# Optimization experiments

Measured on AMD Instinct MI355X. Metric: run time of the kernel, lower is better.

Reference implementation:

```python
import jax, jax.numpy as jnp
import numpy as np

N = 512          # n_nodes
F = 64           # hidden scalar/vector channels (hidden_irreps 64x0e+64x1o)
S = 5            # num_species
T = 32           # time embedding dim
M = 64           # MLP_irreps 64x0e
L = 2            # num_interactions
AVG = 511.0      # avg_num_neighbors (fully connected)
E = N * (N - 1)


def _sph(v):
    """Real spherical harmonics l=0,1,2 (component norm) of normalized vectors. v: [E,3]."""
    r = jnp.linalg.norm(v, axis=-1, keepdims=True)  # [E,1]
    u = v / r
    x, y, z = u[..., 0], u[..., 1], u[..., 2]
    s3, s5, s15 = 3.0 ** 0.5, 5.0 ** 0.5, 15.0 ** 0.5
    Y0 = jnp.ones_like(x)[..., None]
    Y1 = s3 * u
    Y2 = jnp.stack([s15 * x * y, s15 * y * z, 0.5 * s5 * (3 * z * z - 1.0),
                    s15 * x * z, 0.5 * s15 * (x * x - y * y)], axis=-1)
    return jnp.concatenate([Y0, Y1, Y2], axis=-1), r  # [E,9], [E,1]


def setup_inputs() -> dict:
    key = jax.random.key(0)
    ks = jax.random.split(key, 16)
    snd, rcv = np.nonzero(~np.eye(N, dtype=bool))  # fully-connected, no self loops
    return dict(
        positions=jax.random.normal(ks[0], (N, 3), jnp.float32),
        node_features=jax.random.randint(ks[1], (N,), 1, S + 1, jnp.int32),
        time_embedding=jax.random.normal(ks[2], (T,), jnp.float32),
        senders=jnp.asarray(snd, jnp.int32),
        receivers=jnp.asarray(rcv, jnp.int32),
        W_embed=jax.random.normal(ks[3], (S + T, F)) * 0.1,
        b_embed=jnp.zeros((F,)),
        W_lin=jax.random.normal(ks[4], (L, 3, F, F)) / jnp.sqrt(float(F)),
        W_e1=jax.random.normal(ks[5], (L, 1, 32)),
        b_e1=jnp.zeros((L, 32)),
        W_e2=jax.random.normal(ks[6], (L, 32, F * 6)) * 0.05,
        Wp0=jax.random.normal(ks[7], (L, S, F, 6)) * 0.1,
        Wp1=jax.random.normal(ks[8], (L, S, F, 3)) * 0.1,
        Wr1=jax.random.normal(ks[9], (L, F, M)) / jnp.sqrt(float(F)),
        br1=jnp.zeros((L, M)),
        Wr2s=jax.random.normal(ks[10], (L, M, 16)) * 0.1,
        Wr2g=jax.random.normal(ks[11], (L, M, F)) * 0.1,
    )


def reference(positions, node_features, time_embedding, senders, receivers,
              W_embed, b_embed, W_lin, W_e1, b_e1, W_e2, Wp0, Wp1, Wr1, br1, Wr2s, Wr2g):
    species = node_features - 1                                  # ints in [0,S)
    onehot = jax.nn.one_hot(species, S, dtype=positions.dtype)   # /normalization_factor=1
    te = jnp.tile(time_embedding, (N, 1))
    h = jnp.concatenate([onehot, te], axis=-1) @ W_embed + b_embed  # embedding Dense -> [N,F]
    node_feats = jnp.zeros((N, F, 9), positions.dtype).at[:, :, 0].set(h)
    pos0 = positions
    pos = positions
    for l in range(L):
        vec = pos[receivers] - pos[senders]                      # [E,3]
        Y, lengths = _sph(vec)                                   # SH of edge dirs, edge lengths
        # per-l channel-mixing linear on node feats
        x0 = jnp.einsum('nf,fg->ng', node_feats[:, :, 0], W_lin[l, 0])
        x1 = jnp.einsum('nfm,fg->ngm', node_feats[:, :, 1:4], W_lin[l, 1])
        x2 = jnp.einsum('nfm,fg->ngm', node_feats[:, :, 4:9], W_lin[l, 2])
        s0, s1, s2 = x0[senders], x1[senders], x2[senders]       # gather sender feats
        # edge-length MLP producing per-channel per-CG-path weights
        he = jax.nn.silu(lengths @ W_e1[l] + b_e1[l])            # [E,32]
        w = (he @ W_e2[l]).reshape(-1, F, 6)                     # 6 TP paths
        Y1 = Y[:, None, 1:4]
        Y2c = Y[:, None, 4:9]
        # CG tensor-product paths: 0x0->0, 0x1->1, 0x2->2, 1x1->0, 1x1->1, 2x2->0
        m0 = (w[..., 0] * s0 * Y[:, 0:1]
              + w[..., 3] * jnp.sum(s1 * Y1, -1)
              + w[..., 5] * jnp.sum(s2 * Y2c, -1))               # [E,F]
        m1 = w[..., 1, None] * s0[..., None] * Y1 + w[..., 4, None] * jnp.cross(s1, Y1)
        m2 = w[..., 2, None] * s0[..., None] * Y2c
        msg = jnp.concatenate([m0[..., None], m1, m2], axis=-1)  # [E,F,9]
        A = jax.ops.segment_sum(msg, receivers, num_segments=N) / AVG  # scatter-aggregate
        # EquivariantProductBasisBlock: species-weighted symmetric contractions (correlation 3)
        A0, A1, A2 = A[:, :, 0], A[:, :, 1:4], A[:, :, 4:9]
        n1 = jnp.sum(A1 * A1, -1)
        n2 = jnp.sum(A2 * A2, -1)
        t0 = jnp.stack([A0, A0 * A0, A0 ** 3, n1, n2, A0 * n1], axis=-1)
        w0 = Wp0[l][species]                                     # [N,F,6]
        w1 = Wp1[l][species]                                     # [N,F,3]
        out0 = jnp.sum(t0 * w0, -1)                              # [N,F] scalars
        gpoly = w1[..., 0] + w1[..., 1] * A0 + w1[..., 2] * A0 * A0
        out1 = gpoly[..., None] * A1                             # [N,F,3] vectors
        node_feats = (jnp.zeros((N, F, 9), positions.dtype)
                      .at[:, :, 0].set(out0).at[:, :, 1:4].set(out1))
        # NonLinearReadoutBlock: gated vector readout (scalar outputs are discarded upstream)
        hr = jax.nn.silu(out0 @ Wr1[l] + br1[l])
        gate = hr @ Wr2g[l]                                      # [N,F]
        vec_out = jnp.einsum('nf,nfc->nc', gate, out1)           # [N,3] many_body_vectors
        pos = pos + vec_out
    return (pos - pos0)[:, :3]                                    # final_scaling = 1.0
```

## Files before the change

kernel.cpp:

```cpp
#include <hip/hip_runtime.h>
#include <hip/hip_bf16.h>

using bf16 = __hip_bfloat16;
using bf16x8 = __attribute__((ext_vector_type(8))) short;
using f32x4  = __attribute__((ext_vector_type(4))) float;

#define NN 512
#define NS 511

enum : int {
  WS_FLAG = 0,
  WS_POS  = 16,
  WS_POS2 = 1552,
  WS_DELTA= 3088,
  WS_XS0  = 4624,
  WS_XS1  = 135696,
};

__device__ __forceinline__ short f2b(float x) {
  unsigned u = __builtin_bit_cast(unsigned, x);
  unsigned r = (u + 0x7fffu + ((u >> 16) & 1u)) >> 16;
  return (short)r;
}

__device__ __forceinline__ float ld(const void* p, int i, int isf32) {
  if (isf32) return ((const float*)p)[i];
  return __bfloat162float(((const bf16*)p)[i]);
}

__global__ __launch_bounds__(64) void k_pre(
    const void* __restrict__ positions, const int* __restrict__ nodef,
    const void* __restrict__ te, const void* __restrict__ W_embed,
    const void* __restrict__ b_embed, const void* __restrict__ W_lin,
    float* __restrict__ ws) {
  int n = blockIdx.x, f = threadIdx.x;
  int cnt = 0;
  #pragma unroll
  for (int kq = 0; kq < 4; ++kq) {
    float v = __bfloat162float(((const bf16*)W_embed)[f + kq * 64]);
    float av = fabsf(v);
    cnt += (v == v && av > 1e-8f && av < 1e4f) ? 1 : 0;
  }
  #pragma unroll
  for (int off = 32; off > 0; off >>= 1) cnt += __shfl_down(cnt, off);
  int tot = __shfl(cnt, 0);
  int isf32 = (tot >= 240) ? 0 : 1;
  if (n == 0 && f == 0) ((int*)ws)[WS_FLAG] = isf32;

  if (f < 3) ws[WS_POS + n * 3 + f] = ld(positions, n * 3 + f, isf32);

  int sp = nodef[n] - 1;
  float h = ld(b_embed, f, isf32) + ld(W_embed, sp * 64 + f, isf32);
  #pragma unroll 8
  for (int q = 0; q < 32; ++q)
    h += ld(te, q, isf32) * ld(W_embed, (5 + q) * 64 + f, isf32);
  __shared__ float hl[64];
  hl[f] = h;
  __syncthreads();
  float a0 = 0.f;
  #pragma unroll 8
  for (int q = 0; q < 64; ++q)
    a0 += hl[q] * ld(W_lin, q * 64 + f, isf32);
  f32x4 o = {a0, 0.f, 0.f, 0.f};
  *(f32x4*)&ws[WS_XS0 + (n * 64 + f) * 4] = o;
}

template <int L>
__global__ __launch_bounds__(256) void k_edgenode(
    const int* __restrict__ nodef, const void* __restrict__ W_lin,
    const void* __restrict__ W_e1, const void* __restrict__ b_e1,
    const void* __restrict__ W_e2, const void* __restrict__ Wp0,
    const void* __restrict__ Wp1, const void* __restrict__ Wr1,
    const void* __restrict__ br1, const void* __restrict__ Wr2g,
    float* __restrict__ ws, void* __restrict__ out) {
  constexpr int HAS1 = L;
  constexpr int K = HAS1 ? 5 : 3;
  constexpr int N = K * 64;
  const int j = blockIdx.x;
  const int t = threadIdx.x;
  const int lane = t & 63;
  const int wave = t >> 6;
  const int quad = lane >> 4;
  const int lo = lane & 15;

  __shared__ short Bhi[N * 40];
  __shared__ float red[4][64][9];
  __shared__ float Af[64][9];
  __shared__ float s0l[64];
  __shared__ float o1l[3][64];
  __shared__ float hl[64];

  const int isf32 = ((const int*)ws)[WS_FLAG];

  {
    for (int idx = t; idx < N * 32; idx += 256) {
      int n = idx >> 5, h = idx & 31;
      int kp = n >> 6, f = n & 63;
      int src = (L * 32 + h) * 384 + f * 6 + kp;
      short bits;
      if (isf32) bits = f2b(((const float*)W_e2)[src]);
      else       bits = ((const short*)W_e2)[src];
      Bhi[n * 40 + h] = bits;
    }
  }
  const float* pos = ws + (L ? WS_POS2 : WS_POS);
  const f32x4* xs = (const f32x4*)(ws + (L ? WS_XS1 : WS_XS0));
  float we1v[8], be1v[8];
  #pragma unroll
  for (int i = 0; i < 8; ++i) {
    we1v[i] = ld(W_e1, L * 32 + quad * 8 + i, isf32);
    be1v[i] = ld(b_e1, L * 32 + quad * 8 + i, isf32);
  }
  const float pjx = pos[j * 3 + 0], pjy = pos[j * 3 + 1], pjz = pos[j * 3 + 2];

  const float s3 = 1.7320508075688772f;
  const float s5h = 1.118033988749895f;
  const float s15 = 3.872983346207417f;
  const float s15h = 1.9364916731037085f;

  float acc[9][4] = {};
  __syncthreads();

  #pragma unroll 1
  for (int stile = wave; stile < 32; stile += 4) {
    bf16x8 af;
    {
      int ida = stile * 16 + lo;
      int ia = ida + (ida >= j);
      if (ia > 511) ia = 511;
      float pix = pos[ia * 3 + 0], piy = pos[ia * 3 + 1], piz = pos[ia * 3 + 2];
      float vx = pjx - pix, vy = pjy - piy, vz = pjz - piz;
      float r = sqrtf(vx * vx + vy * vy + vz * vz);
      #pragma unroll
      for (int i = 0; i < 8; ++i) {
        float x = r * we1v[i] + be1v[i];
        float he = x / (1.f + __expf(-x));
        af[i] = f2b(he);
      }
    }
    float Y1r[4][3], Y2r[4][5];
    int ir[4];
    bool vld[4];
    #pragma unroll
    for (int r4 = 0; r4 < 4; ++r4) {
      int idx = stile * 16 + quad * 4 + r4;
      vld[r4] = idx < NS;
      int i = idx + (idx >= j);
      if (i > 511) i = 511;
      ir[r4] = i;
      float pix = pos[i * 3 + 0], piy = pos[i * 3 + 1], piz = pos[i * 3 + 2];
      float vx = pjx - pix, vy = pjy - piy, vz = pjz - piz;
      float r2 = vx * vx + vy * vy + vz * vz;
      float rinv = r2 > 0.f ? rsqrtf(r2) : 0.f;
      float ux = vx * rinv, uy = vy * rinv, uz = vz * rinv;
      Y1r[r4][0] = s3 * ux; Y1r[r4][1] = s3 * uy; Y1r[r4][2] = s3 * uz;
      Y2r[r4][0] = s15 * ux * uy;
      Y2r[r4][1] = s15 * uy * uz;
      Y2r[r4][2] = s5h * (3.f * uz * uz - 1.f);
      Y2r[r4][3] = s15 * ux * uz;
      Y2r[r4][4] = s15h * (ux * ux - uy * uy);
    }
    #pragma unroll
    for (int ft = 0; ft < 4; ++ft) {
      int fcol = ft * 16 + lo;
      f32x4 xv[4];
      #pragma unroll
      for (int r4 = 0; r4 < 4; ++r4) xv[r4] = xs[ir[r4] * 64 + fcol];
      f32x4 C[K];
      #pragma unroll
      for (int kp = 0; kp < K; ++kp) {
        const bf16x8 bh = *(const bf16x8*)&Bhi[(kp * 64 + fcol) * 40 + quad * 8];
        f32x4 c = {0.f, 0.f, 0.f, 0.f};
        C[kp] = __builtin_amdgcn_mfma_f32_16x16x32_bf16(af, bh, c, 0, 0, 0);
      }
      #pragma unroll
      for (int r4 = 0; r4 < 4; ++r4) {
        if (vld[r4]) {
          float s0 = xv[r4].x;
          float w0 = C[0][r4], w1 = C[1][r4], w2 = C[2][r4];
          if (HAS1) {
            float s1x = xv[r4].y, s1y = xv[r4].z, s1z = xv[r4].w;
            float w3 = C[3][r4], w4 = C[4][r4];
            float d1 = s1x * Y1r[r4][0] + s1y * Y1r[r4][1] + s1z * Y1r[r4][2];
            float cx = s1y * Y1r[r4][2] - s1z * Y1r[r4][1];
            float cy = s1z * Y1r[r4][0] - s1x * Y1r[r4][2];
            float cz = s1x * Y1r[r4][1] - s1y * Y1r[r4][0];
            acc[0][ft] += w0 * s0 + w3 * d1;
            float t1 = w1 * s0;
            acc[1][ft] += t1 * Y1r[r4][0] + w4 * cx;
            acc[2][ft] += t1 * Y1r[r4][1] + w4 * cy;
            acc[3][ft] += t1 * Y1r[r4][2] + w4 * cz;
          } else {
            acc[0][ft] += w0 * s0;
            float t1 = w1 * s0;
            acc[1][ft] += t1 * Y1r[r4][0];
            acc[2][ft] += t1 * Y1r[r4][1];
            acc[3][ft] += t1 * Y1r[r4][2];
          }
          float t2 = w2 * s0;
          acc[4][ft] += t2 * Y2r[r4][0];
          acc[5][ft] += t2 * Y2r[r4][1];
          acc[6][ft] += t2 * Y2r[r4][2];
          acc[7][ft] += t2 * Y2r[r4][3];
          acc[8][ft] += t2 * Y2r[r4][4];
        }
      }
    }
  }

  #pragma unroll
  for (int c = 0; c < 9; ++c)
    #pragma unroll
    for (int ft = 0; ft < 4; ++ft) {
      float v = acc[c][ft];
      v += __shfl_xor(v, 16);
      v += __shfl_xor(v, 32);
      acc[c][ft] = v;
    }
  if (quad == 0) {
    #pragma unroll
    for (int c = 0; c < 9; ++c)
      #pragma unroll
      for (int ft = 0; ft < 4; ++ft)
        red[wave][ft * 16 + lo][c] = acc[c][ft];
  }
  __syncthreads();
  for (int o = t; o < 576; o += 256) {
    int f = o / 9, c = o % 9;
    Af[f][c] = (red[0][f][c] + red[1][f][c] + red[2][f][c] + red[3][f][c]) *
               (1.f / 511.f);
  }
  __syncthreads();

  float out0 = 0.f, o1x = 0.f, o1y = 0.f, o1z = 0.f;
  if (t < 64) {
    int f = t;
    float a[9];
    #pragma unroll
    for (int c = 0; c < 9; ++c) a[c] = Af[f][c];
    int sp = nodef[j] - 1;
    int b0i = ((L * 5 + sp) * 64 + f) * 6;
    int b1i = ((L * 5 + sp) * 64 + f) * 3;
    float A0 = a[0];
    float n1 = a[1] * a[1] + a[2] * a[2] + a[3] * a[3];
    float n2 = a[4] * a[4] + a[5] * a[5] + a[6] * a[6] + a[7] * a[7] + a[8] * a[8];
    float A02 = A0 * A0;
    out0 = ld(Wp0, b0i + 0, isf32) * A0 + ld(Wp0, b0i + 1, isf32) * A02 +
           ld(Wp0, b0i + 2, isf32) * A02 * A0 + ld(Wp0, b0i + 3, isf32) * n1 +
           ld(Wp0, b0i + 4, isf32) * n2 + ld(Wp0, b0i + 5, isf32) * A0 * n1;
    float gp = ld(Wp1, b1i + 0, isf32) + ld(Wp1, b1i + 1, isf32) * A0 +
               ld(Wp1, b1i + 2, isf32) * A02;
    o1x = gp * a[1]; o1y = gp * a[2]; o1z = gp * a[3];
    s0l[f] = out0;
    if (L == 0) { o1l[0][f] = o1x; o1l[1][f] = o1y; o1l[2][f] = o1z; }
  }
  __syncthreads();
  if (t < 64) {
    int f = t;
    if (L == 0) {
      float b0 = 0.f, bx = 0.f, by = 0.f, bz = 0.f;
      #pragma unroll 8
      for (int q = 0; q < 64; ++q) {
        float w0 = ld(W_lin, 3 * 4096 + q * 64 + f, isf32);
        float w1 = ld(W_lin, 4 * 4096 + q * 64 + f, isf32);
        b0 += s0l[q] * w0;
        bx += o1l[0][q] * w1; by += o1l[1][q] * w1; bz += o1l[2][q] * w1;
      }
      f32x4 o = {b0, bx, by, bz};
      *(f32x4*)&ws[WS_XS1 + (j * 64 + f) * 4] = o;
    }
    float hacc = ld(br1, L * 64 + f, isf32);
    #pragma unroll 8
    for (int q = 0; q < 64; ++q)
      hacc += s0l[q] * ld(Wr1, (L * 64 + q) * 64 + f, isf32);
    hl[f] = hacc / (1.f + __expf(-hacc));
  }
  __syncthreads();
  if (t < 64) {
    int f = t;
    float gacc = 0.f;
    #pragma unroll 8
    for (int m = 0; m < 64; ++m)
      gacc += hl[m] * ld(Wr2g, (L * 64 + m) * 64 + f, isf32);
    float px = gacc * o1x, py = gacc * o1y, pz = gacc * o1z;
    #pragma unroll
    for (int off = 32; off > 0; off >>= 1) {
      px += __shfl_down(px, off);
      py += __shfl_down(py, off);
      pz += __shfl_down(pz, off);
    }
    if (f == 0) {
      if (L == 0) {
        ws[WS_DELTA + j * 3 + 0] = px;
        ws[WS_DELTA + j * 3 + 1] = py;
        ws[WS_DELTA + j * 3 + 2] = pz;
        ws[WS_POS2 + j * 3 + 0] = pos[j * 3 + 0] + px;
        ws[WS_POS2 + j * 3 + 1] = pos[j * 3 + 1] + py;
        ws[WS_POS2 + j * 3 + 2] = pos[j * 3 + 2] + pz;
      } else {
        float ox = ws[WS_DELTA + j * 3 + 0] + px;
        float oy = ws[WS_DELTA + j * 3 + 1] + py;
        float oz = ws[WS_DELTA + j * 3 + 2] + pz;
        if (isf32) {
          float* o = (float*)out;
          o[j * 3 + 0] = ox; o[j * 3 + 1] = oy; o[j * 3 + 2] = oz;
        } else {
          bf16* o = (bf16*)out;
          o[j * 3 + 0] = __float2bfloat16(ox);
          o[j * 3 + 1] = __float2bfloat16(oy);
          o[j * 3 + 2] = __float2bfloat16(oz);
        }
      }
    }
  }
}

extern "C" void kernel_launch(void* const* d_in, const int* in_sizes, int n_in,
                              void* d_out, int out_size, void* d_ws, size_t ws_size,
                              hipStream_t stream) {
  const void* positions = d_in[0];
  const int*  nodef     = (const int*)d_in[1];
  const void* te        = d_in[2];
  const void* W_embed   = d_in[5];
  const void* b_embed   = d_in[6];
  const void* W_lin     = d_in[7];
  const void* W_e1      = d_in[8];
  const void* b_e1      = d_in[9];
  const void* W_e2      = d_in[10];
  const void* Wp0       = d_in[11];
  const void* Wp1       = d_in[12];
  const void* Wr1       = d_in[13];
  const void* br1       = d_in[14];
  const void* Wr2g      = d_in[16];
  float* ws = (float*)d_ws;
  (void)in_sizes; (void)n_in; (void)out_size; (void)ws_size;

  k_pre<<<dim3(512), dim3(64), 0, stream>>>(positions, nodef, te, W_embed,
                                            b_embed, W_lin, ws);
  k_edgenode<0><<<dim3(512), dim3(256), 0, stream>>>(
      nodef, W_lin, W_e1, b_e1, W_e2, Wp0, Wp1, Wr1, br1, Wr2g, ws, d_out);
  k_edgenode<1><<<dim3(512), dim3(256), 0, stream>>>(
      nodef, W_lin, W_e1, b_e1, W_e2, Wp0, Wp1, Wr1, br1, Wr2g, ws, d_out);
}
```

Measured before the change: 207.7 us.

## Compute layer-0 node features per species instead of per node

```diff
diff --git a/kernel.cpp b/kernel.cpp
--- a/kernel.cpp
+++ b/kernel.cpp
@@ -10,11 +10,11 @@
 
 enum : int {
   WS_FLAG = 0,
-  WS_POS  = 16,
-  WS_POS2 = 1552,
-  WS_DELTA= 3088,
-  WS_XS0  = 4624,
-  WS_XS1  = 135696,
+  WS_X0S  = 16,
+  WS_POS  = 336,
+  WS_POS2 = 1872,
+  WS_DELTA= 3408,
+  WS_XS1  = 4960,
 };
 
 __device__ __forceinline__ short f2b(float x) {
@@ -28,41 +28,55 @@
   return __bfloat162float(((const bf16*)p)[i]);
 }
 
-__global__ __launch_bounds__(64) void k_pre(
-    const void* __restrict__ positions, const int* __restrict__ nodef,
-    const void* __restrict__ te, const void* __restrict__ W_embed,
-    const void* __restrict__ b_embed, const void* __restrict__ W_lin,
-    float* __restrict__ ws) {
-  int n = blockIdx.x, f = threadIdx.x;
-  int cnt = 0;
-  #pragma unroll
-  for (int kq = 0; kq < 4; ++kq) {
-    float v = __bfloat162float(((const bf16*)W_embed)[f + kq * 64]);
-    float av = fabsf(v);
-    cnt += (v == v && av > 1e-8f && av < 1e4f) ? 1 : 0;
-  }
-  #pragma unroll
-  for (int off = 32; off > 0; off >>= 1) cnt += __shfl_down(cnt, off);
-  int tot = __shfl(cnt, 0);
-  int isf32 = (tot >= 240) ? 0 : 1;
-  if (n == 0 && f == 0) ((int*)ws)[WS_FLAG] = isf32;
-
-  if (f < 3) ws[WS_POS + n * 3 + f] = ld(positions, n * 3 + f, isf32);
-
-  int sp = nodef[n] - 1;
-  float h = ld(b_embed, f, isf32) + ld(W_embed, sp * 64 + f, isf32);
-  #pragma unroll 8
-  for (int q = 0; q < 32; ++q)
-    h += ld(te, q, isf32) * ld(W_embed, (5 + q) * 64 + f, isf32);
-  __shared__ float hl[64];
-  hl[f] = h;
-  __syncthreads();
-  float a0 = 0.f;
-  #pragma unroll 8
-  for (int q = 0; q < 64; ++q)
-    a0 += hl[q] * ld(W_lin, q * 64 + f, isf32);
-  f32x4 o = {a0, 0.f, 0.f, 0.f};
-  *(f32x4*)&ws[WS_XS0 + (n * 64 + f) * 4] = o;
+__global__ __launch_bounds__(320) void k_pre(
+    const void* __restrict__ positions, const void* __restrict__ te,
+    const void* __restrict__ W_embed, const void* __restrict__ b_embed,
+    const void* __restrict__ W_lin, float* __restrict__ ws) {
+  const int t = threadIdx.x;
+  __shared__ int flag_s;
+  __shared__ float hst[5][64];
+  if (t < 64) {
+    int cnt = 0;
+    #pragma unroll
+    for (int kq = 0; kq < 4; ++kq) {
+      float v = __bfloat162float(((const bf16*)W_embed)[t + kq * 64]);
+      float av = fabsf(v);
+      cnt += (v == v && av > 1e-8f && av < 1e4f) ? 1 : 0;
+    }
+    #pragma unroll
+    for (int off = 32; off > 0; off >>= 1) cnt += __shfl_down(cnt, off);
+    if (t == 0) {
+      int isf32 = (cnt >= 240) ? 0 : 1;
+      flag_s = isf32;
+      ((int*)ws)[WS_FLAG] = isf32;
+    }
+  }
+  __syncthreads();
+  const int isf32 = flag_s;
+  for (int idx = t; idx < NN * 3; idx += 320)
+    ws[WS_POS + idx] = ld(positions, idx, isf32);
+  __shared__ float tv[64];
+  if (t < 64) {
+    float s = ld(b_embed, t, isf32);
+    #pragma unroll 8
+    for (int q = 0; q < 32; ++q)
+      s += ld(te, q, isf32) * ld(W_embed, (5 + q) * 64 + t, isf32);
+    tv[t] = s;
+  }
+  __syncthreads();
+  {
+    int sp = t >> 6, q = t & 63;
+    hst[sp][q] = tv[q] + ld(W_embed, sp * 64 + q, isf32);
+  }
+  __syncthreads();
+  {
+    int sp = t >> 6, f = t & 63;
+    float a0 = 0.f;
+    #pragma unroll 8
+    for (int q = 0; q < 64; ++q)
+      a0 += hst[sp][q] * ld(W_lin, q * 64 + f, isf32);
+    ws[WS_X0S + sp * 64 + f] = a0;
+  }
 }
 
 template <int L>
@@ -89,6 +103,7 @@
   __shared__ float s0l[64];
   __shared__ float o1l[3][64];
   __shared__ float hl[64];
+  __shared__ float X0l[320];
 
   const int isf32 = ((const int*)ws)[WS_FLAG];
 
@@ -102,9 +117,12 @@
       else       bits = ((const short*)W_e2)[src];
       Bhi[n * 40 + h] = bits;
     }
+    if (!HAS1) {
+      for (int idx = t; idx < 320; idx += 256) X0l[idx] = ws[WS_X0S + idx];
+    }
   }
   const float* pos = ws + (L ? WS_POS2 : WS_POS);
-  const f32x4* xs = (const f32x4*)(ws + (L ? WS_XS1 : WS_XS0));
+  const f32x4* xs = (const f32x4*)(ws + WS_XS1);
   float we1v[8], be1v[8];
   #pragma unroll
   for (int i = 0; i < 8; ++i) {
@@ -139,7 +157,7 @@
       }
     }
     float Y1r[4][3], Y2r[4][5];
-    int ir[4];
+    int ir[4], sp4[4];
     bool vld[4];
     #pragma unroll
     for (int r4 = 0; r4 < 4; ++r4) {
@@ -148,6 +166,7 @@
       int i = idx + (idx >= j);
       if (i > 511) i = 511;
       ir[r4] = i;
+      if (!HAS1) sp4[r4] = nodef[i] - 1;
       float pix = pos[i * 3 + 0], piy = pos[i * 3 + 1], piz = pos[i * 3 + 2];
       float vx = pjx - pix, vy = pjy - piy, vz = pjz - piz;
       float r2 = vx * vx + vy * vy + vz * vz;
@@ -164,8 +183,16 @@
     for (int ft = 0; ft < 4; ++ft) {
       int fcol = ft * 16 + lo;
       f32x4 xv[4];
-      #pragma unroll
-      for (int r4 = 0; r4 < 4; ++r4) xv[r4] = xs[ir[r4] * 64 + fcol];
+      if (HAS1) {
+        #pragma unroll
+        for (int r4 = 0; r4 < 4; ++r4) xv[r4] = xs[ir[r4] * 64 + fcol];
+      } else {
+        #pragma unroll
+        for (int r4 = 0; r4 < 4; ++r4) {
+          f32x4 v = {X0l[sp4[r4] * 64 + fcol], 0.f, 0.f, 0.f};
+          xv[r4] = v;
+        }
+      }
       f32x4 C[K];
       #pragma unroll
       for (int kp = 0; kp < K; ++kp) {
@@ -335,8 +362,8 @@
   float* ws = (float*)d_ws;
   (void)in_sizes; (void)n_in; (void)out_size; (void)ws_size;
 
-  k_pre<<<dim3(512), dim3(64), 0, stream>>>(positions, nodef, te, W_embed,
-                                            b_embed, W_lin, ws);
+  k_pre<<<dim3(1), dim3(320), 0, stream>>>(positions, te, W_embed, b_embed,
+                                           W_lin, ws);
   k_edgenode<0><<<dim3(512), dim3(256), 0, stream>>>(
       nodef, W_lin, W_e1, b_e1, W_e2, Wp0, Wp1, Wr1, br1, Wr2g, ws, d_out);
   k_edgenode<1><<<dim3(512), dim3(256), 0, stream>>>(
```

After: 194.0 us. 6.6% less time.
